# Kernel tuning notes

Measured on AMD Instinct MI355X. Metric: run time of the kernel, lower is better.

The kernel has to match this reference:

```python
import jax, jax.numpy as jnp
import numpy as np

BN_EPS = 1e-5


def setup_inputs() -> dict:
    key = jax.random.key(0)
    ks = jax.random.split(key, 9)
    b, c, h, w = 8, 256, 256, 25
    p2_r = jax.random.normal(ks[0], (b, c, h, w), dtype=jnp.float32)
    # message-passing conv weight; scaled so the 25-step recurrence stays bounded
    W_msg = jax.random.normal(ks[1], (256, 256, 1, 9), dtype=jnp.float32) * 0.02
    bn_gamma = jax.random.uniform(ks[2], (256,), dtype=jnp.float32, minval=0.5, maxval=1.5)
    bn_beta = jax.random.normal(ks[3], (256,), dtype=jnp.float32) * 0.1
    bn_mean = jax.random.normal(ks[4], (256,), dtype=jnp.float32) * 0.1
    bn_var = jax.random.uniform(ks[5], (256,), dtype=jnp.float32, minval=0.5, maxval=1.5)
    W_up2 = jax.random.normal(ks[6], (256, 256, 3, 3), dtype=jnp.float32) * (1.0 / np.sqrt(256 * 9))
    W_conv = jax.random.normal(ks[7], (1, 256, 1, 1), dtype=jnp.float32) * (1.0 / np.sqrt(256))
    W_conv2 = jax.random.normal(ks[8], (1, 25, 1, 1), dtype=jnp.float32) * (1.0 / np.sqrt(25))
    return {"p2_r": p2_r, "W_msg": W_msg, "bn_gamma": bn_gamma, "bn_beta": bn_beta,
            "bn_mean": bn_mean, "bn_var": bn_var, "W_up2": W_up2,
            "W_conv": W_conv, "W_conv2": W_conv2}


def r_scnn(x, Wc, reverse):
    # x: [b,c,h,w]. The (1,9) conv with padding (0,4) on width-1 slices only
    # touches the kernel's center tap -> per-step 256x256 matvec recurrence.
    xs = jnp.moveaxis(x, 3, 0)  # [w,b,c,h]
    if reverse:
        xs = xs[::-1]

    def step(carry, xi):
        new = xi + jax.nn.relu(jnp.einsum('oc,bch->boh', Wc, carry))
        return new, new

    _, rest = jax.lax.scan(step, xs[0], xs[1:])
    out = jnp.concatenate([xs[:1], rest], axis=0)[::-1]  # source reverses output order
    return jnp.moveaxis(out, 0, 3)  # [b,c,h,w]


def batchnorm(x, gamma, beta, mean, var):
    inv = gamma / jnp.sqrt(var + BN_EPS)
    return x * inv[None, :, None, None] + (beta - mean * inv)[None, :, None, None]


def upsample_h2(x):
    # bilinear, align_corners=True, size=(2H, W): only height doubles
    b, c, H, W = x.shape
    nh = 2 * H
    pos = jnp.arange(nh, dtype=jnp.float32) * ((H - 1) / (nh - 1))
    i0 = jnp.floor(pos).astype(jnp.int32)
    i1 = jnp.minimum(i0 + 1, H - 1)
    t = (pos - i0.astype(jnp.float32))[None, None, :, None]
    return x[:, :, i0, :] * (1.0 - t) + x[:, :, i1, :] * t


def reference(p2_r, W_msg, bn_gamma, bn_beta, bn_mean, bn_var, W_up2, W_conv, W_conv2):
    Wc = W_msg[:, :, 0, 4]  # effective center tap of the (1,9) conv
    x = r_scnn(p2_r, Wc, reverse=False)
    x = jax.nn.relu(batchnorm(x, bn_gamma, bn_beta, bn_mean, bn_var))
    x = r_scnn(x, Wc, reverse=True)
    x = jax.nn.relu(batchnorm(x, bn_gamma, bn_beta, bn_mean, bn_var))
    x = upsample_h2(x)  # [b,256,2h,w]
    x = jax.lax.conv_general_dilated(x, W_up2, (1, 1), ((1, 1), (1, 1)),
                                     dimension_numbers=('NCHW', 'OIHW', 'NCHW'))
    x = upsample_h2(x)  # [b,256,4h,w]
    x = jnp.einsum('oc,bchw->bohw', W_conv[:, :, 0, 0], x)  # 1x1 conv 256->1
    x = upsample_h2(x)  # [b,1,8h,w]
    x = jnp.swapaxes(x, 1, 3)  # [b,w,8h,1]
    x = jnp.einsum('oc,bchw->bohw', W_conv2[:, :, 0, 0], x)  # 1x1 conv 25->1
    return jax.nn.sigmoid(x)  # [b,1,8h,1]
```

## Files before the change

kernel.cpp:

```cpp
#include <hip/hip_runtime.h>
#include <math.h>


#define NC 8

typedef __attribute__((ext_vector_type(8))) short bf16x8;
typedef __attribute__((ext_vector_type(4))) float f32x4;

__device__ __forceinline__ float relu_(float v) { return fmaxf(v, 0.f); }

__device__ __forceinline__ short f2bf(float f) {
  union { float f; unsigned u; } v; v.f = f;
  unsigned r = (v.u + 0x7fffu + ((v.u >> 16) & 1u)) >> 16;
  return (short)r;
}
__device__ __forceinline__ float bf2f(short s) {
  union { unsigned u; float f; } v;
  v.u = ((unsigned)(unsigned short)s) << 16;
  return v.f;
}
__device__ __forceinline__ unsigned cvtpk(float lo, float hi) {
  unsigned r;
  asm("v_cvt_pk_bf16_f32 %0, %1, %2" : "=v"(r) : "v"(lo), "v"(hi));
  return r;
}
__device__ __forceinline__ float dpp_xor8(float v) {
  int r = __builtin_amdgcn_update_dpp(0, __float_as_int(v), 0x128, 0xf, 0xf, true);
  return __int_as_float(r);
}

__global__ __launch_bounds__(64) void k0_precompute(
    const float* __restrict__ Wmsg, const float* __restrict__ gamma,
    const float* __restrict__ beta, const float* __restrict__ mean,
    const float* __restrict__ var, const float* __restrict__ Wup2,
    const float* __restrict__ Wconv, const float* __restrict__ Wconv2,
    short* __restrict__ WcA, float* __restrict__ A, float* __restrict__ bnp)
{
  const int c = blockIdx.x;
  const int lane = threadIdx.x;

  for (int o = lane; o < 256; o += 64)
    WcA[o * 256 + c] = f2bf(Wmsg[(o * 256 + c) * 9 + 4]);

  const int gtid = c * 64 + lane;
  if (gtid < 256) {
    float inv = gamma[gtid] / sqrtf(var[gtid] + 1e-5f);
    bnp[gtid] = inv;
    bnp[256 + gtid] = beta[gtid] - mean[gtid] * inv;
  }

  float wacc[9];
#pragma unroll
  for (int q = 0; q < 9; ++q) wacc[q] = 0.f;
  for (int o = lane; o < 256; o += 64) {
    float cw = Wconv[o];
    const float* wp = Wup2 + (size_t)(o * 256 + c) * 9;
#pragma unroll
    for (int q = 0; q < 9; ++q) wacc[q] += cw * wp[q];
  }
#pragma unroll
  for (int q = 0; q < 9; ++q) {
    float v = wacc[q];
    v += __shfl_xor(v, 32, 64);
    v += __shfl_xor(v, 16, 64);
    v += __shfl_xor(v, 8, 64);
    v += __shfl_xor(v, 4, 64);
    v += __shfl_xor(v, 2, 64);
    v += __shfl_xor(v, 1, 64);
    wacc[q] = v;
  }
  if (lane == 0) {
    for (int dh = 0; dh < 3; ++dh)
      for (int j = 0; j < 25; ++j) {
        float a = 0.f;
        for (int dw = 0; dw < 3; ++dw) {
          int w = j + 1 - dw;
          if (w >= 0 && w < 25) a += wacc[dh * 3 + dw] * Wconv2[w];
        }
        A[(dh * 25 + j) * 256 + c] = a;
      }
  }
}

__global__ __launch_bounds__(256) void k2a_pack(
    const float* __restrict__ X, char* __restrict__ xG)
{
  __shared__ short xslab[25 * 8 * 256];
  const int tid = threadIdx.x;
  const int wave = tid >> 6;
  const int lane = tid & 63;
  const int col0 = blockIdx.x * NC;
  const int b = col0 >> 8, h0 = col0 & 255;
  const int obase = wave * 64;
  char* xs = (char*)xslab;

  if (lane < 50) {
    int base_[4], sx_[4];
#pragma unroll
    for (int e = 0; e < 4; ++e) {
      int f = 4 * lane + e;
      int rn = f / 25, w = f - rn * 25;
      base_[e] = w * 4096 + rn * 512;
      sx_[e] = ((2 * rn + w) & 15) << 3;
    }
    const float* src0 = X + (size_t)(b * 256 + obase) * 6400 + h0 * 25 + 4 * lane;
#pragma unroll 4
    for (int i = 0; i < 32; ++i) {
      float4 v0 = *(const float4*)(src0 + (size_t)(2 * i) * 6400);
      float4 v1 = *(const float4*)(src0 + (size_t)(2 * i + 1) * 6400);
      unsigned p[4] = {cvtpk(v0.x, v1.x), cvtpk(v0.y, v1.y),
                       cvtpk(v0.z, v1.z), cvtpk(v0.w, v1.w)};
      const int cb = 2 * obase + 4 * i;
#pragma unroll
      for (int e = 0; e < 4; ++e)
        *(unsigned*)(xs + base_[e] + (cb ^ sx_[e])) = p[e];
    }
  }
  __syncthreads();

  const uint4* src = (const uint4*)xs;
  uint4* dst = (uint4*)(xG + (size_t)blockIdx.x * 102400);
#pragma unroll
  for (int i = 0; i < 25; ++i)
    dst[i * 256 + tid] = src[i * 256 + tid];
}

__global__ __launch_bounds__(512, 1) void k2b_loop(
    const char* __restrict__ xG,
    const short* __restrict__ WcA,
    const float* __restrict__ A,
    const float* __restrict__ bnp,
    float* __restrict__ S)
{
  __shared__ short xslab[25 * 8 * 256];
  __shared__ short yz[2][16 * 256];
  __shared__ float red[8][8][3];
  const int tid = threadIdx.x;
  const int wave = tid >> 6;
  const int lane = tid & 63;
  const int n = lane & 15;
  const int nr = n & 7;
  const int g = lane >> 4;
  const bool isz = (n >= 8);
  const int col0 = blockIdx.x * NC;
  const int obase = wave * 32;
  char* xs = (char*)xslab;
  char* smem = (char*)yz;

  {
    const uint4* gsrc = (const uint4*)(xG + (size_t)blockIdx.x * 102400);
    uint4* ldst = (uint4*)xs;
    for (int i = tid; i < 6400; i += 512) ldst[i] = gsrc[i];
  }

  f32x4 inv[2], addv[2];
#pragma unroll
  for (int t = 0; t < 2; ++t) {
    inv[t] = *(const f32x4*)(bnp + obase + t * 16 + g * 4);
    addv[t] = *(const f32x4*)(bnp + 256 + obase + t * 16 + g * 4);
  }

  bf16x8 af[2][8];
#pragma unroll
  for (int t = 0; t < 2; ++t)
#pragma unroll
    for (int kk = 0; kk < 8; ++kk)
      af[t][kk] = *(const bf16x8*)(WcA + (obase + t * 16 + n) * 256 + kk * 32 + g * 8);

  const int swz = nr << 4;
  int woff[2], xb[2], roff[8];
#pragma unroll
  for (int t = 0; t < 2; ++t) {
    woff[t] = n * 512 + (((obase + t * 16 + g * 4) * 2) ^ swz);
    xb[t] = nr * 512 + 2 * (obase + t * 16 + g * 4);
  }
#pragma unroll
  for (int kk = 0; kk < 8; ++kk)
    roff[kk] = n * 512 + ((kk * 64 + g * 16) ^ swz);

  __syncthreads();

  {
    const int S0 = ((2 * nr) & 15) << 3;
#pragma unroll
    for (int t = 0; t < 2; ++t) {
      uint2 xq0 = *(const uint2*)(xs + (xb[t] ^ S0));
      if (!isz) {
        *(uint2*)(smem + woff[t]) = xq0;
      } else {
        float zr[4], t2r[4];
        float xv[4] = {bf2f((short)xq0.x), bf2f((short)(xq0.x >> 16)),
                       bf2f((short)xq0.y), bf2f((short)(xq0.y >> 16))};
#pragma unroll
        for (int r = 0; r < 4; ++r) {
          zr[r] = relu_(xv[r] * inv[t][r] + addv[t][r]);
          t2r[r] = relu_(zr[r] * inv[t][r] + addv[t][r]);
        }
        *(uint2*)(smem + woff[t]) = make_uint2(cvtpk(zr[0], zr[1]), cvtpk(zr[2], zr[3]));
        *(uint2*)(xs + (xb[t] ^ S0)) =
            make_uint2(cvtpk(t2r[0], t2r[1]), cvtpk(t2r[2], t2r[3]));
      }
    }
  }

  uint2 xq[2];
  xq[0] = make_uint2(0u, 0u);
  xq[1] = make_uint2(0u, 0u);
  if (!isz) {
    const int S1 = ((2 * nr + 1) & 15) << 3;
#pragma unroll
    for (int t = 0; t < 2; ++t)
      xq[t] = *(const uint2*)(xs + ((xb[t] + 4096) ^ S1));
  }
  __syncthreads();

#pragma unroll 1
  for (int k = 1; k < 25; ++k) {
    const int cur = (k - 1) & 1, nxt = k & 1;

    bf16x8 bfr[8];
#pragma unroll
    for (int kk = 0; kk < 8; ++kk)
      bfr[kk] = *(const bf16x8*)(smem + cur * 8192 + roff[kk]);

    f32x4 accA[2], accB[2];
#pragma unroll
    for (int t = 0; t < 2; ++t) {
      accA[t] = (f32x4){0.f, 0.f, 0.f, 0.f};
      accB[t] = (f32x4){0.f, 0.f, 0.f, 0.f};
    }
#pragma unroll
    for (int kk = 0; kk < 4; ++kk)
#pragma unroll
      for (int t = 0; t < 2; ++t)
        accA[t] = __builtin_amdgcn_mfma_f32_16x16x32_bf16(af[t][kk], bfr[kk], accA[t], 0, 0, 0);
#pragma unroll
    for (int kk = 4; kk < 8; ++kk)
#pragma unroll
      for (int t = 0; t < 2; ++t)
        accB[t] = __builtin_amdgcn_mfma_f32_16x16x32_bf16(af[t][kk], bfr[kk], accB[t], 0, 0, 0);

    float cyv[2][4], ynv[2][4], t1v[2][4], t1s[2][4];
#pragma unroll
    for (int t = 0; t < 2; ++t) {
      f32x4 acc = accA[t] + accB[t];
      float xv[4];
      xv[0] = bf2f((short)xq[t].x);
      xv[1] = bf2f((short)(xq[t].x >> 16));
      xv[2] = bf2f((short)xq[t].y);
      xv[3] = bf2f((short)(xq[t].y >> 16));
#pragma unroll
      for (int r = 0; r < 4; ++r) {
        cyv[t][r] = relu_(acc[r]);
        ynv[t][r] = xv[r] + cyv[t][r];
        t1v[t][r] = relu_(ynv[t][r] * inv[t][r] + addv[t][r]);
      }
    }
#pragma unroll
    for (int t = 0; t < 2; ++t)
#pragma unroll
      for (int r = 0; r < 4; ++r) t1s[t][r] = dpp_xor8(t1v[t][r]);
#pragma unroll
    for (int t = 0; t < 2; ++t) {
      float sel[4], tt2[4];
#pragma unroll
      for (int r = 0; r < 4; ++r) {
        float znew = t1s[t][r] + cyv[t][r];
        tt2[r] = relu_(znew * inv[t][r] + addv[t][r]);
        sel[r] = isz ? znew : ynv[t][r];
      }
      *(uint2*)(smem + nxt * 8192 + woff[t]) =
          make_uint2(cvtpk(sel[0], sel[1]), cvtpk(sel[2], sel[3]));
      if (isz)
        *(uint2*)(xs + ((xb[t] + k * 4096) ^ (((2 * nr + k) & 15) << 3))) =
            make_uint2(cvtpk(tt2[0], tt2[1]), cvtpk(tt2[2], tt2[3]));
    }

    if (k < 24 && !isz) {
      const int Sn = ((2 * nr + k + 1) & 15) << 3;
#pragma unroll
      for (int t = 0; t < 2; ++t)
        xq[t] = *(const uint2*)(xs + ((xb[t] + (k + 1) * 4096) ^ Sn));
    }
    __syncthreads();
  }

  {
    const int kb = (wave == 0) ? 0 : 4 + 3 * (wave - 1);
    const int ke = kb + (wave ? 3 : 4);
    float acc[8][3];
#pragma unroll
    for (int rn = 0; rn < 8; ++rn)
#pragma unroll
      for (int dh = 0; dh < 3; ++dh) acc[rn][dh] = 0.f;

#pragma unroll 1
    for (int k = kb; k < ke; ++k) {
      f32x4 a0 = *(const f32x4*)(A + (0 * 25 + 24 - k) * 256 + 4 * lane);
      f32x4 a1 = *(const f32x4*)(A + (1 * 25 + 24 - k) * 256 + 4 * lane);
      f32x4 a2 = *(const f32x4*)(A + (2 * 25 + 24 - k) * 256 + 4 * lane);
#pragma unroll
      for (int rn = 0; rn < 8; ++rn) {
        int Sp = ((2 * rn + k) & 15) << 3;
        uint2 q = *(const uint2*)(xs + ((k * 4096 + rn * 512 + 8 * lane) ^ Sp));
        float v0 = bf2f((short)q.x), v1 = bf2f((short)(q.x >> 16));
        float v2 = bf2f((short)q.y), v3 = bf2f((short)(q.y >> 16));
#pragma unroll
        for (int dh = 0; dh < 3; ++dh) {
          f32x4 a = dh == 0 ? a0 : (dh == 1 ? a1 : a2);
          float s = acc[rn][dh];
          s = fmaf(a[0], v0, s);
          s = fmaf(a[1], v1, s);
          s = fmaf(a[2], v2, s);
          s = fmaf(a[3], v3, s);
          acc[rn][dh] = s;
        }
      }
    }
#pragma unroll
    for (int rn = 0; rn < 8; ++rn)
#pragma unroll
      for (int dh = 0; dh < 3; ++dh) {
        float v = acc[rn][dh];
        v += __shfl_xor(v, 1);
        v += __shfl_xor(v, 2);
        v += __shfl_xor(v, 4);
        v += __shfl_xor(v, 8);
        v += __shfl_xor(v, 16);
        v += __shfl_xor(v, 32);
        if (lane == 0) red[wave][rn][dh] = v;
      }
  }
  __syncthreads();
  if (tid < 24) {
    int nn = tid / 3, dh = tid % 3;
    float v = 0.f;
#pragma unroll
    for (int ww = 0; ww < 8; ++ww) v += red[ww][nn][dh];
    S[(size_t)(col0 + nn) * 3 + dh] = v;
  }
}

__global__ __launch_bounds__(256) void k3_outpre(
    const float* __restrict__ S, float* __restrict__ P)
{
  int idx = blockIdx.x * blockDim.x + threadIdx.x;
  if (idx >= 8 * 512) return;
  int b = idx >> 9, h = idx & 511;
  float acc = 0.f;
#pragma unroll
  for (int dh = 0; dh < 3; ++dh) {
    int hh = h + dh - 1;
    if (hh < 0 || hh >= 512) continue;
    float pos = hh * (255.0f / 511.0f);
    int i0 = (int)floorf(pos);
    int i1 = min(i0 + 1, 255);
    float t = pos - (float)i0;
    acc += (1.f - t) * S[(size_t)(b * 256 + i0) * 3 + dh]
         + t * S[(size_t)(b * 256 + i1) * 3 + dh];
  }
  P[idx] = acc;
}

__global__ __launch_bounds__(256) void k4_final(
    const float* __restrict__ P, float* __restrict__ out)
{
  int idx = blockIdx.x * blockDim.x + threadIdx.x;
  if (idx >= 8 * 2048) return;
  int b = idx >> 11, H = idx & 2047;
  const float* Pb = P + b * 512;

  float pos3 = H * (1023.0f / 2047.0f);
  int i3 = (int)floorf(pos3);
  int i3b = min(i3 + 1, 1023);
  float t3 = pos3 - (float)i3;

  float v[2];
#pragma unroll
  for (int q = 0; q < 2; ++q) {
    int i = q ? i3b : i3;
    float pos2 = i * (511.0f / 1023.0f);
    int i2 = (int)floorf(pos2);
    int i2b = min(i2 + 1, 511);
    float t2 = pos2 - (float)i2;
    v[q] = (1.f - t2) * Pb[i2] + t2 * Pb[i2b];
  }
  float val = (1.f - t3) * v[0] + t3 * v[1];
  out[idx] = 1.f / (1.f + expf(-val));
}

extern "C" void kernel_launch(void* const* d_in, const int* in_sizes, int n_in,
                              void* d_out, int out_size, void* d_ws, size_t ws_size,
                              hipStream_t stream) {
  (void)in_sizes; (void)n_in; (void)out_size; (void)ws_size;
  const float* p2r    = (const float*)d_in[0];
  const float* Wmsg   = (const float*)d_in[1];
  const float* gamma  = (const float*)d_in[2];
  const float* beta   = (const float*)d_in[3];
  const float* mean   = (const float*)d_in[4];
  const float* var    = (const float*)d_in[5];
  const float* Wup2   = (const float*)d_in[6];
  const float* Wconv  = (const float*)d_in[7];
  const float* Wconv2 = (const float*)d_in[8];
  float* out = (float*)d_out;

  float* ws = (float*)d_ws;
  size_t off = 0;
  char* xG = (char*)(ws + off); off += 6553600;
  short* WcA = (short*)(ws + off); off += 32768;
  float* Abuf = ws + off; off += 19200;
  float* bnp = ws + off;  off += 512;
  float* S = ws + off;    off += 6144;
  float* P = ws + off;    off += 4096;

  k0_precompute<<<256, 64, 0, stream>>>(Wmsg, gamma, beta, mean, var, Wup2,
                                        Wconv, Wconv2, WcA, Abuf, bnp);
  k2a_pack<<<256, 256, 0, stream>>>(p2r, xG);
  k2b_loop<<<256, 512, 0, stream>>>(xG, (const short*)WcA, Abuf, bnp, S);
  k3_outpre<<<16, 256, 0, stream>>>(S, P);
  k4_final<<<64, 256, 0, stream>>>(P, out);
}
```

Baseline: 63.37 us.

## Fuse input packing into recurrence kernel and merge output upsample kernels

Packs p2_r into bf16 swizzled LDS directly inside the recurrence kernel, removing the separate pack kernel and its global round-trip through a workspace buffer. The two final upsample kernels are merged so the intermediate P is recomputed from S on the fly, and MFMA sections get raised wave priority with s_setprio. This cuts two launches and about 26MB of global traffic, at the cost of redundant interpolation math in the final kernel. With 512 threads (8 waves each handling 32 channels), the pack loop shortens to 16 iterations.

After: 52.98 us. -16.4%, faster.

```diff
diff --git a/kernel.cpp b/kernel.cpp
--- a/kernel.cpp
+++ b/kernel.cpp
@@ -82,51 +82,8 @@
   }
 }
 
-__global__ __launch_bounds__(256) void k2a_pack(
-    const float* __restrict__ X, char* __restrict__ xG)
-{
-  __shared__ short xslab[25 * 8 * 256];
-  const int tid = threadIdx.x;
-  const int wave = tid >> 6;
-  const int lane = tid & 63;
-  const int col0 = blockIdx.x * NC;
-  const int b = col0 >> 8, h0 = col0 & 255;
-  const int obase = wave * 64;
-  char* xs = (char*)xslab;
-
-  if (lane < 50) {
-    int base_[4], sx_[4];
-#pragma unroll
-    for (int e = 0; e < 4; ++e) {
-      int f = 4 * lane + e;
-      int rn = f / 25, w = f - rn * 25;
-      base_[e] = w * 4096 + rn * 512;
-      sx_[e] = ((2 * rn + w) & 15) << 3;
-    }
-    const float* src0 = X + (size_t)(b * 256 + obase) * 6400 + h0 * 25 + 4 * lane;
-#pragma unroll 4
-    for (int i = 0; i < 32; ++i) {
-      float4 v0 = *(const float4*)(src0 + (size_t)(2 * i) * 6400);
-      float4 v1 = *(const float4*)(src0 + (size_t)(2 * i + 1) * 6400);
-      unsigned p[4] = {cvtpk(v0.x, v1.x), cvtpk(v0.y, v1.y),
-                       cvtpk(v0.z, v1.z), cvtpk(v0.w, v1.w)};
-      const int cb = 2 * obase + 4 * i;
-#pragma unroll
-      for (int e = 0; e < 4; ++e)
-        *(unsigned*)(xs + base_[e] + (cb ^ sx_[e])) = p[e];
-    }
-  }
-  __syncthreads();
-
-  const uint4* src = (const uint4*)xs;
-  uint4* dst = (uint4*)(xG + (size_t)blockIdx.x * 102400);
-#pragma unroll
-  for (int i = 0; i < 25; ++i)
-    dst[i * 256 + tid] = src[i * 256 + tid];
-}
-
-__global__ __launch_bounds__(512, 1) void k2b_loop(
-    const char* __restrict__ xG,
+__global__ __launch_bounds__(512, 1) void k2_fused(
+    const float* __restrict__ X,
     const short* __restrict__ WcA,
     const float* __restrict__ A,
     const float* __restrict__ bnp,
@@ -143,14 +100,32 @@
   const int g = lane >> 4;
   const bool isz = (n >= 8);
   const int col0 = blockIdx.x * NC;
+  const int b = col0 >> 8, h0 = col0 & 255;
   const int obase = wave * 32;
   char* xs = (char*)xslab;
   char* smem = (char*)yz;
 
-  {
-    const uint4* gsrc = (const uint4*)(xG + (size_t)blockIdx.x * 102400);
-    uint4* ldst = (uint4*)xs;
-    for (int i = tid; i < 6400; i += 512) ldst[i] = gsrc[i];
+  if (lane < 50) {
+    int base_[4], sx_[4];
+#pragma unroll
+    for (int e = 0; e < 4; ++e) {
+      int f = 4 * lane + e;
+      int rn = f / 25, w = f - rn * 25;
+      base_[e] = w * 4096 + rn * 512;
+      sx_[e] = ((2 * rn + w) & 15) << 3;
+    }
+    const float* src0 = X + (size_t)(b * 256 + obase) * 6400 + h0 * 25 + 4 * lane;
+#pragma unroll 4
+    for (int i = 0; i < 16; ++i) {
+      float4 v0 = *(const float4*)(src0 + (size_t)(2 * i) * 6400);
+      float4 v1 = *(const float4*)(src0 + (size_t)(2 * i + 1) * 6400);
+      unsigned p[4] = {cvtpk(v0.x, v1.x), cvtpk(v0.y, v1.y),
+                       cvtpk(v0.z, v1.z), cvtpk(v0.w, v1.w)};
+      const int cb = 2 * obase + 4 * i;
+#pragma unroll
+      for (int e = 0; e < 4; ++e)
+        *(unsigned*)(xs + base_[e] + (cb ^ sx_[e])) = p[e];
+    }
   }
 
   f32x4 inv[2], addv[2];
@@ -229,6 +204,7 @@
       accA[t] = (f32x4){0.f, 0.f, 0.f, 0.f};
       accB[t] = (f32x4){0.f, 0.f, 0.f, 0.f};
     }
+    __builtin_amdgcn_s_setprio(1);
 #pragma unroll
     for (int kk = 0; kk < 4; ++kk)
 #pragma unroll
@@ -239,6 +215,7 @@
 #pragma unroll
       for (int t = 0; t < 2; ++t)
         accB[t] = __builtin_amdgcn_mfma_f32_16x16x32_bf16(af[t][kk], bfr[kk], accB[t], 0, 0, 0);
+    __builtin_amdgcn_s_setprio(0);
 
     float cyv[2][4], ynv[2][4], t1v[2][4], t1s[2][4];
 #pragma unroll
@@ -341,34 +318,28 @@
   }
 }
 
-__global__ __launch_bounds__(256) void k3_outpre(
-    const float* __restrict__ S, float* __restrict__ P)
-{
-  int idx = blockIdx.x * blockDim.x + threadIdx.x;
-  if (idx >= 8 * 512) return;
-  int b = idx >> 9, h = idx & 511;
-  float acc = 0.f;
-#pragma unroll
-  for (int dh = 0; dh < 3; ++dh) {
-    int hh = h + dh - 1;
-    if (hh < 0 || hh >= 512) continue;
-    float pos = hh * (255.0f / 511.0f);
-    int i0 = (int)floorf(pos);
-    int i1 = min(i0 + 1, 255);
-    float t = pos - (float)i0;
-    acc += (1.f - t) * S[(size_t)(b * 256 + i0) * 3 + dh]
-         + t * S[(size_t)(b * 256 + i1) * 3 + dh];
-  }
-  P[idx] = acc;
-}
-
-__global__ __launch_bounds__(256) void k4_final(
-    const float* __restrict__ P, float* __restrict__ out)
+__global__ __launch_bounds__(256) void k34_final(
+    const float* __restrict__ S, float* __restrict__ out)
 {
   int idx = blockIdx.x * blockDim.x + threadIdx.x;
   if (idx >= 8 * 2048) return;
   int b = idx >> 11, H = idx & 2047;
-  const float* Pb = P + b * 512;
+
+  auto Pf = [&](int h) -> float {
+    float acc = 0.f;
+#pragma unroll
+    for (int dh = 0; dh < 3; ++dh) {
+      int hh = h + dh - 1;
+      if (hh < 0 || hh >= 512) continue;
+      float pos = hh * (255.0f / 511.0f);
+      int i0 = (int)floorf(pos);
+      int i1 = min(i0 + 1, 255);
+      float t = pos - (float)i0;
+      acc += (1.f - t) * S[(size_t)(b * 256 + i0) * 3 + dh]
+           + t * S[(size_t)(b * 256 + i1) * 3 + dh];
+    }
+    return acc;
+  };
 
   float pos3 = H * (1023.0f / 2047.0f);
   int i3 = (int)floorf(pos3);
@@ -383,7 +354,7 @@
     int i2 = (int)floorf(pos2);
     int i2b = min(i2 + 1, 511);
     float t2 = pos2 - (float)i2;
-    v[q] = (1.f - t2) * Pb[i2] + t2 * Pb[i2b];
+    v[q] = (1.f - t2) * Pf(i2) + t2 * Pf(i2b);
   }
   float val = (1.f - t3) * v[0] + t3 * v[1];
   out[idx] = 1.f / (1.f + expf(-val));
@@ -406,17 +377,13 @@
 
   float* ws = (float*)d_ws;
   size_t off = 0;
-  char* xG = (char*)(ws + off); off += 6553600;
   short* WcA = (short*)(ws + off); off += 32768;
   float* Abuf = ws + off; off += 19200;
   float* bnp = ws + off;  off += 512;
   float* S = ws + off;    off += 6144;
-  float* P = ws + off;    off += 4096;
 
   k0_precompute<<<256, 64, 0, stream>>>(Wmsg, gamma, beta, mean, var, Wup2,
                                         Wconv, Wconv2, WcA, Abuf, bnp);
-  k2a_pack<<<256, 256, 0, stream>>>(p2r, xG);
-  k2b_loop<<<256, 512, 0, stream>>>(xG, (const short*)WcA, Abuf, bnp, S);
-  k3_outpre<<<16, 256, 0, stream>>>(S, P);
-  k4_final<<<64, 256, 0, stream>>>(P, out);
-}
+  k2_fused<<<256, 512, 0, stream>>>(p2r, (const short*)WcA, Abuf, bnp, S);
+  k34_final<<<64, 256, 0, stream>>>(S, out);
+}
```
